# Optimization experiments

Measured on AMD Instinct MI355X. Metric: run time of the kernel, lower is better.

The kernel has to match this reference:

```python
import jax, jax.numpy as jnp
import numpy as np

N_NODES = 50000
N_EDGES = 600000
NUM_ENTITIES = 50000
EMBED = 128
HIDDEN = 128
NUM_TYPES = 16


def setup_inputs() -> dict:
    key = jax.random.key(0)
    ks = jax.random.split(key, 12)
    entity = jax.random.randint(ks[0], (N_NODES,), 0, NUM_ENTITIES, dtype=jnp.int64 if jax.config.jax_enable_x64 else jnp.int32)
    edge_index = jax.random.randint(ks[1], (2, N_EDGES), 0, N_NODES, dtype=jnp.int32)
    s = 1.0 / np.sqrt(EMBED)
    emb = jax.random.normal(ks[2], (NUM_ENTITIES, EMBED), jnp.float32)
    emb = emb.at[0].set(0.0)  # padding_idx=0
    W1_l = jax.random.uniform(ks[3], (EMBED, HIDDEN), jnp.float32, -s, s)
    b1 = jax.random.uniform(ks[4], (HIDDEN,), jnp.float32, -s, s)
    W1_r = jax.random.uniform(ks[5], (EMBED, HIDDEN), jnp.float32, -s, s)
    W2_l = jax.random.uniform(ks[6], (HIDDEN, HIDDEN), jnp.float32, -s, s)
    b2 = jax.random.uniform(ks[7], (HIDDEN,), jnp.float32, -s, s)
    W2_r = jax.random.uniform(ks[8], (HIDDEN, HIDDEN), jnp.float32, -s, s)
    Wc = jax.random.uniform(ks[9], (HIDDEN, NUM_TYPES), jnp.float32, -s, s)
    bc = jax.random.uniform(ks[10], (NUM_TYPES,), jnp.float32, -s, s)
    return {"entity": entity, "edge_index": edge_index, "emb": emb,
            "W1_l": W1_l, "b1": b1, "W1_r": W1_r,
            "W2_l": W2_l, "b2": b2, "W2_r": W2_r,
            "Wc": Wc, "bc": bc}


def _sage_conv(x, src, dst, Wl, bl, Wr):
    # PyG SAGEConv (aggr='mean'): out = lin_l(mean_{j->i} x_j) + lin_r(x_i)
    msgs = x[src]                                            # [E, D] gather
    agg = jax.ops.segment_sum(msgs, dst, num_segments=N_NODES)
    deg = jax.ops.segment_sum(jnp.ones((src.shape[0],), x.dtype), dst, num_segments=N_NODES)
    agg = agg / jnp.maximum(deg, 1.0)[:, None]               # mean; 0 for isolated nodes
    return agg @ Wl + bl + x @ Wr


def reference(entity, edge_index, emb, W1_l, b1, W1_r, W2_l, b2, W2_r, Wc, bc):
    src, dst = edge_index[0], edge_index[1]
    x = emb[entity]                                          # [N, 128] embedding lookup
    x = jax.nn.relu(_sage_conv(x, src, dst, W1_l, b1, W1_r))
    x = _sage_conv(x, src, dst, W2_l, b2, W2_r)
    return x @ Wc + bc                                       # [N, num_node_types]
```

## Files before the change

### kernel.cpp

```cpp
#include <hip/hip_runtime.h>

typedef _Float16 half4  __attribute__((ext_vector_type(4)));
typedef _Float16 half8  __attribute__((ext_vector_type(8)));
typedef float    f32x4  __attribute__((ext_vector_type(4)));

#define EC 768
#define CAP 4096
#define CHUNK 2048
#define CPAD 16
#define GA_PER 4

__device__ __forceinline__ void gather_unit(const int* __restrict__ ent,
                                            const float* __restrict__ emb,
                                            _Float16* __restrict__ X,
                                            int unit, int lt, int N) {
  int t = unit * 256 + lt;
  if (t >= N * 16) return;
  int node = t >> 4, g = t & 15;
  const float4* s = (const float4*)(emb + (long)ent[node] * 128 + g * 8);
  float4 a = s[0], c = s[1];
  half8 o;
  o[0] = (_Float16)a.x; o[1] = (_Float16)a.y; o[2] = (_Float16)a.z; o[3] = (_Float16)a.w;
  o[4] = (_Float16)c.x; o[5] = (_Float16)c.y; o[6] = (_Float16)c.z; o[7] = (_Float16)c.w;
  *(half8*)(X + (long)t * 8) = o;
}

__device__ __forceinline__ void pack_dev(const float* Wa, const float* Wb,
                                         _Float16* out, int NT, int ncols, int t) {
  int lane = t & 63, tile = t >> 6;
  int nt = tile % NT, kt = tile / NT;
  int n  = nt * 16 + (lane & 15);
  int kb = kt * 32 + (lane >> 4) * 8;
  half8 o;
#pragma unroll
  for (int j = 0; j < 8; ++j) {
    int k = kb + j;
    float w = (k < 128) ? Wa[k * ncols + n] : Wb[(k - 128) * ncols + n];
    o[j] = (_Float16)w;
  }
  *(half8*)(out + (long)t * 8) = o;
}

__global__ __launch_bounds__(256) void bucketA_k(
    const int* __restrict__ src, const int* __restrict__ dst,
    int* __restrict__ cur, int* __restrict__ buck,
    const int* __restrict__ ent, const float* __restrict__ emb, _Float16* __restrict__ X,
    const float* __restrict__ W1l, const float* __restrict__ W1r, _Float16* __restrict__ Wp1,
    const float* __restrict__ W2l, const float* __restrict__ W2r, const float* __restrict__ Wc,
    _Float16* __restrict__ Wz, const float* __restrict__ b2, const float* __restrict__ bc,
    float* __restrict__ bpr, int N, int E, int NA, int NBUCK, int IBA) {
  int b = blockIdx.x;
  if (b < IBA) {
    int grp = b / (GA_PER + 1), ph = b % (GA_PER + 1);
    if (ph != 0) { gather_unit(ent, emb, X, grp * GA_PER + ph - 1, threadIdx.x, N); return; }
    __shared__ int lbin[256], gbase[256];
    int tl = threadIdx.x;
    lbin[tl] = 0; __syncthreads();
    int e0 = grp * CHUNK;
    int pk[8], bn[8], lr[8];
    if (e0 + CHUNK <= E) {
      const int4* dp = (const int4*)(dst + e0 + tl * 8);
      const int4* sp = (const int4*)(src + e0 + tl * 8);
      int4 d0 = dp[0], d1 = dp[1], s0 = sp[0], s1 = sp[1];
      int dv[8] = {d0.x, d0.y, d0.z, d0.w, d1.x, d1.y, d1.z, d1.w};
      int sv[8] = {s0.x, s0.y, s0.z, s0.w, s1.x, s1.y, s1.z, s1.w};
#pragma unroll
      for (int k = 0; k < 8; ++k) {
        bn[k] = dv[k] >> 8;
        pk[k] = (sv[k] << 8) | (dv[k] & 255);
        lr[k] = atomicAdd(&lbin[bn[k]], 1);
      }
    } else {
#pragma unroll
      for (int k = 0; k < 8; ++k) {
        int e = e0 + tl * 8 + k;
        bn[k] = -1;
        if (e < E) {
          int d = dst[e];
          bn[k] = d >> 8;
          pk[k] = (src[e] << 8) | (d & 255);
          lr[k] = atomicAdd(&lbin[bn[k]], 1);
        }
      }
    }
    __syncthreads();
    gbase[tl] = (tl < NBUCK && lbin[tl]) ? atomicAdd(&cur[tl * CPAD], lbin[tl]) : 0;
    __syncthreads();
#pragma unroll
    for (int k = 0; k < 8; ++k) {
      if (bn[k] >= 0) {
        int idx = gbase[bn[k]] + lr[k];
        if (idx < CAP) buck[(long)bn[k] * CAP + idx] = pk[k];
      }
    }
  } else if (b < IBA + 16) {
    pack_dev(W1l, W1r, Wp1, 8, 128, (b - IBA) * 256 + threadIdx.x);
  } else if (b < IBA + 32) {
    int i = (b - IBA - 16) * 256 + threadIdx.x;
    int j = i & 7, lane = (i >> 3) & 63, tile = i >> 9;
    int nt = tile & 1, kt = tile >> 1;
    int k = kt * 32 + (lane >> 4) * 8 + j;
    int c = lane & 15;
    const float* W = nt ? W2r : W2l;
    float s = 0.f;
#pragma unroll 8
    for (int q = 0; q < 128; ++q) s += W[k * 128 + q] * Wc[q * 16 + c];
    Wz[i] = (_Float16)s;
  } else {
    int n = threadIdx.x;
    if (n < 16) {
      float s = bc[n];
      for (int k = 0; k < 128; ++k) s += b2[k] * Wc[k * 16 + n];
      bpr[n] = s;
    }
  }
}

__global__ __launch_bounds__(512) void bucketB_k(
    const int* __restrict__ cur, const int* __restrict__ buck,
    int* __restrict__ row_off, int* __restrict__ csr,
    const int* __restrict__ ent, const float* __restrict__ emb,
    _Float16* __restrict__ X, int goff, int N, int E, int NBUCK) {
  int B0 = blockIdx.x, tl = threadIdx.x;
  if (B0 >= NBUCK) {
    int unit = goff + (B0 - NBUCK) * 2 + (tl >> 8);
    gather_unit(ent, emb, X, unit, tl & 255, N);
    return;
  }
  __shared__ int sA[256], cnt[256], sB[256], run[256];
  if (tl < 256) sA[tl] = (tl < NBUCK) ? cur[tl * CPAD] : 0;
  if (tl < 256) cnt[tl] = 0;
  __syncthreads();
  for (int off = 1; off < 256; off <<= 1) {
    int a = (tl < 256) ? sA[tl] : 0;
    int bb = (tl >= off && tl < 256) ? sA[tl - off] : 0;
    __syncthreads();
    if (tl < 256) sA[tl] = a + bb;
    __syncthreads();
  }
  int bsz = cur[B0 * CPAD]; if (bsz > CAP) bsz = CAP;
  int ebase = sA[B0] - bsz;
  const int* bp = buck + (long)B0 * CAP;
  for (int i = tl; i < bsz; i += 512) atomicAdd(&cnt[bp[i] & 255], 1);
  __syncthreads();
  int cv = (tl < 256) ? cnt[tl] : 0;
  if (tl < 256) sB[tl] = cv;
  __syncthreads();
  for (int off = 1; off < 256; off <<= 1) {
    int a = (tl < 256) ? sB[tl] : 0;
    int bb = (tl >= off && tl < 256) ? sB[tl - off] : 0;
    __syncthreads();
    if (tl < 256) sB[tl] = a + bb;
    __syncthreads();
  }
  if (tl < 256) {
    int loff = sB[tl] - cv;
    int node = (B0 << 8) + tl;
    if (node < N) row_off[node] = ebase + loff;
    if (B0 == 0 && tl == 0) row_off[N] = E;
    run[tl] = loff;
  }
  __syncthreads();
  for (int i = tl; i < bsz; i += 512) {
    int w = bp[i];
    int r = atomicAdd(&run[w & 255], 1);
    csr[ebase + r] = w >> 8;
  }
}

__device__ __forceinline__ void agg_to_lds(const _Float16* __restrict__ X,
                                           const int* __restrict__ row_off,
                                           const int* __restrict__ csr,
                                           _Float16* ab, int* eidx,
                                           int row0, int M, int lane) {
  int nd_end = min(row0 + 16, M);
  int ebeg = row_off[row0 < M ? row0 : M - 1];
  int eend = row_off[nd_end];
  int cnt  = eend - ebeg;
  bool fits = (cnt <= EC);
  if (fits)
    for (int i = lane; i < cnt; i += 64) eidx[i] = csr[ebeg + i];
  int g = lane >> 4, j = lane & 15;
#pragma unroll
  for (int batch = 0; batch < 4; ++batch) {
    int node = row0 + batch * 4 + g;
    int nc = (node < M) ? node : M - 1;
    int beg = row_off[nc], end = row_off[nc + 1];
    half8 acc = (half8)(_Float16)0.f;
    if (fits) {
      const int* ix = eidx + (beg - ebeg);
      int n = end - beg;
#pragma unroll 8
      for (int e = 0; e < n; ++e) {
        half8 v = *(const half8*)(X + (long)ix[e] * 128 + j * 8);
        acc += v;
      }
    } else {
#pragma unroll 8
      for (int e = beg; e < end; ++e) {
        half8 v = *(const half8*)(X + (long)csr[e] * 128 + j * 8);
        acc += v;
      }
    }
    _Float16 inv = (_Float16)(1.f / fmaxf((float)(end - beg), 1.f));
    acc *= (half8)inv;
    *(half8*)(ab + (batch * 4 + g) * 136 + j * 8) = acc;
  }
}

__global__ __launch_bounds__(128) void gemm1z_k(const _Float16* __restrict__ X,
                                                const int* __restrict__ row_off,
                                                const int* __restrict__ csr,
                                                const _Float16* __restrict__ Bp,
                                                const float* __restrict__ bias,
                                                const _Float16* __restrict__ Bz,
                                                const float* __restrict__ bprime,
                                                _Float16* __restrict__ Zl,
                                                float* __restrict__ Pr, int M) {
  __shared__ _Float16 abuf[2][16 * 136];
  __shared__ int      ebuf[2][EC];
  int wave = threadIdx.x >> 6, lane = threadIdx.x & 63;
  _Float16* ab = abuf[wave];
  int row0 = blockIdx.x * 32 + wave * 16;
  agg_to_lds(X, row_off, csr, ab, ebuf[wave], row0, M, lane);
  int m = lane & 15, quad = lane >> 4;
  int arow = row0 + m; if (arow > M - 1) arow = M - 1;
  f32x4 acc[8];
#pragma unroll
  for (int i = 0; i < 8; ++i) acc[i] = (f32x4){0.f, 0.f, 0.f, 0.f};
#pragma unroll
  for (int kt = 0; kt < 8; ++kt) {
    half8 af = (kt < 4) ? *(const half8*)(ab + m * 136 + kt * 32 + quad * 8)
                        : *(const half8*)(X + (long)arow * 128 + (kt - 4) * 32 + quad * 8);
    __builtin_amdgcn_s_setprio(1);
#pragma unroll
    for (int nt = 0; nt < 8; ++nt) {
      half8 bf = *(const half8*)(Bp + ((long)(kt * 8 + nt) * 64 + lane) * 8);
      acc[nt] = __builtin_amdgcn_mfma_f32_16x16x32_f16(af, bf, acc[nt], 0, 0, 0);
    }
    __builtin_amdgcn_s_setprio(0);
  }
#pragma unroll
  for (int nt = 0; nt < 8; ++nt) {
    float bv = bias[nt * 16 + m];
#pragma unroll
    for (int r = 0; r < 4; ++r)
      ab[(quad * 4 + r) * 136 + nt * 16 + m] = (_Float16)fmaxf(acc[nt][r] + bv, 0.f);
  }
  f32x4 a0 = (f32x4){0.f, 0.f, 0.f, 0.f}, a1 = a0;
  __builtin_amdgcn_s_setprio(1);
#pragma unroll
  for (int kt = 0; kt < 4; ++kt) {
    half8 af = *(const half8*)(ab + m * 136 + kt * 32 + quad * 8);
    half8 b0 = *(const half8*)(Bz + ((long)(kt * 2 + 0) * 64 + lane) * 8);
    half8 b1 = *(const half8*)(Bz + ((long)(kt * 2 + 1) * 64 + lane) * 8);
    a0 = __builtin_amdgcn_mfma_f32_16x16x32_f16(af, b0, a0, 0, 0, 0);
    a1 = __builtin_amdgcn_mfma_f32_16x16x32_f16(af, b1, a1, 0, 0, 0);
  }
  __builtin_amdgcn_s_setprio(0);
  float bv = bprime[m];
#pragma unroll
  for (int r = 0; r < 4; ++r) {
    int orow = row0 + quad * 4 + r;
    if (orow < M) {
      Zl[(long)orow * 16 + m] = (_Float16)a0[r];
      Pr[(long)orow * 16 + m] = a1[r] + bv;
    }
  }
}

__global__ __launch_bounds__(256) void aggout_k(const _Float16* __restrict__ Zl,
                                                const float* __restrict__ Pr,
                                                const int* __restrict__ row_off,
                                                const int* __restrict__ csr,
                                                float* __restrict__ out, int M) {
  int t = blockIdx.x * 256 + threadIdx.x;
  int node = t >> 2, q = t & 3;
  if (node >= M) return;
  int beg = row_off[node], end = row_off[node + 1];
  float a0 = 0.f, a1 = 0.f, a2 = 0.f, a3 = 0.f;
#pragma unroll 8
  for (int e = beg; e < end; ++e) {
    half4 v = *(const half4*)(Zl + (long)csr[e] * 16 + q * 4);
    a0 += (float)v[0]; a1 += (float)v[1]; a2 += (float)v[2]; a3 += (float)v[3];
  }
  float inv = 1.f / fmaxf((float)(end - beg), 1.f);
  long o = (long)node * 16 + q * 4;
  const float4 pv = *(const float4*)(Pr + o);
  float4 ov;
  ov.x = a0 * inv + pv.x; ov.y = a1 * inv + pv.y;
  ov.z = a2 * inv + pv.z; ov.w = a3 * inv + pv.w;
  *(float4*)(out + o) = ov;
}

extern "C" void kernel_launch(void* const* d_in, const int* in_sizes, int n_in,
                              void* d_out, int out_size, void* d_ws, size_t ws_size,
                              hipStream_t stream) {
  const int N = in_sizes[0];
  const int E = in_sizes[1] / 2;
  const int*   entity = (const int*)d_in[0];
  const int*   e_src  = (const int*)d_in[1];
  const int*   e_dst  = e_src + E;
  const float* emb    = (const float*)d_in[2];
  const float* W1l    = (const float*)d_in[3];
  const float* b1     = (const float*)d_in[4];
  const float* W1r    = (const float*)d_in[5];
  const float* W2l    = (const float*)d_in[6];
  const float* b2     = (const float*)d_in[7];
  const float* W2r    = (const float*)d_in[8];
  const float* Wc     = (const float*)d_in[9];
  const float* bc     = (const float*)d_in[10];
  float* out = (float*)d_out;

  const int NBUCK = (N + 255) >> 8;

  char* p = (char*)d_ws;
  _Float16* x0  = (_Float16*)p; p += (size_t)N * 128 * 2;
  _Float16* Wp1 = (_Float16*)p; p += 256 * 128 * 2;
  _Float16* Wz  = (_Float16*)p; p += 128 * 32 * 2;
  float*    bpr = (float*)p;    p += 16 * 4;
  _Float16* Zl  = (_Float16*)p; p += (size_t)N * 16 * 2;
  float*    Pr  = (float*)p;    p += (size_t)N * 16 * 4;
  int* cur     = (int*)p; p += (size_t)NBUCK * CPAD * 4;
  int* row_off = (int*)p; p += (size_t)(N + 1) * 4;
  int* csr     = (int*)p; p += (size_t)E * 4;
  int* buck    = (int*)p; p += (size_t)NBUCK * CAP * 4;

  const int NA  = (E + CHUNK - 1) / CHUNK;
  const int GB  = (N * 16 + 255) / 256;
  const int IBA = (GA_PER + 1) * NA;
  int G1 = NA * GA_PER; if (G1 > GB) G1 = GB;
  const int G2 = GB - G1;
  const int BG = (G2 + 1) / 2;

  hipMemsetAsync(cur, 0, (size_t)NBUCK * CPAD * 4, stream);

  bucketA_k<<<IBA + 33, 256, 0, stream>>>(e_src, e_dst, cur, buck,
                                          entity, emb, x0, W1l, W1r, Wp1,
                                          W2l, W2r, Wc, Wz, b2, bc, bpr,
                                          N, E, NA, NBUCK, IBA);
  bucketB_k<<<NBUCK + BG, 512, 0, stream>>>(cur, buck, row_off, csr,
                                            entity, emb, x0, G1, N, E, NBUCK);
  gemm1z_k<<<(N + 31) / 32, 128, 0, stream>>>(x0, row_off, csr, Wp1, b1,
                                              Wz, bpr, Zl, Pr, N);
  aggout_k<<<(N * 4 + 255) / 256, 256, 0, stream>>>(Zl, Pr, row_off, csr, out, N);
}
```

Before: 156.1 us.

## Split gemm1z block work across four waves sharing LDS tiles

The fused aggregate+GEMM kernel now uses 256 threads per 32-row block instead of 128. Each of four waves aggregates 8 rows, then the waves form a 2x2 grid over rows and output columns for the MFMA stages. LDS tiles are shared through __syncthreads, and the ebuf region is reused for the hidden activations. This halves per-wave accumulator registers and gives more latency-hiding parallelism during the gather, at the cost of two block barriers.

```diff
diff --git a/kernel.cpp b/kernel.cpp
--- a/kernel.cpp
+++ b/kernel.cpp
@@ -168,22 +168,23 @@
   }
 }
 
-__device__ __forceinline__ void agg_to_lds(const _Float16* __restrict__ X,
-                                           const int* __restrict__ row_off,
-                                           const int* __restrict__ csr,
-                                           _Float16* ab, int* eidx,
-                                           int row0, int M, int lane) {
-  int nd_end = min(row0 + 16, M);
-  int ebeg = row_off[row0 < M ? row0 : M - 1];
-  int eend = row_off[nd_end];
+__device__ __forceinline__ void agg8(const _Float16* __restrict__ X,
+                                     const int* __restrict__ row_off,
+                                     const int* __restrict__ csr,
+                                     _Float16* ab,
+                                     int* eidx,
+                                     int rowbase, int M, int lane) {
+  int rb0 = rowbase < M ? rowbase : M - 1;
+  int rb1 = rowbase + 8; if (rb1 > M) rb1 = M;
+  int ebeg = row_off[rb0], eend = row_off[rb1];
   int cnt  = eend - ebeg;
   bool fits = (cnt <= EC);
   if (fits)
     for (int i = lane; i < cnt; i += 64) eidx[i] = csr[ebeg + i];
   int g = lane >> 4, j = lane & 15;
 #pragma unroll
-  for (int batch = 0; batch < 4; ++batch) {
-    int node = row0 + batch * 4 + g;
+  for (int batch = 0; batch < 2; ++batch) {
+    int node = rowbase + batch * 4 + g;
     int nc = (node < M) ? node : M - 1;
     int beg = row_off[nc], end = row_off[nc + 1];
     half8 acc = (half8)(_Float16)0.f;
@@ -208,7 +209,7 @@
   }
 }
 
-__global__ __launch_bounds__(128) void gemm1z_k(const _Float16* __restrict__ X,
+__global__ __launch_bounds__(256) void gemm1z_k(const _Float16* __restrict__ X,
                                                 const int* __restrict__ row_off,
                                                 const int* __restrict__ csr,
                                                 const _Float16* __restrict__ Bp,
@@ -217,54 +218,58 @@
                                                 const float* __restrict__ bprime,
                                                 _Float16* __restrict__ Zl,
                                                 float* __restrict__ Pr, int M) {
-  __shared__ _Float16 abuf[2][16 * 136];
-  __shared__ int      ebuf[2][EC];
+  __shared__ _Float16 abuf[32 * 136];
+  __shared__ int      ebuf_raw[4 * EC];
+  _Float16* h1b = (_Float16*)ebuf_raw;
   int wave = threadIdx.x >> 6, lane = threadIdx.x & 63;
-  _Float16* ab = abuf[wave];
-  int row0 = blockIdx.x * 32 + wave * 16;
-  agg_to_lds(X, row_off, csr, ab, ebuf[wave], row0, M, lane);
+  int row0 = blockIdx.x * 32;
+  agg8(X, row_off, csr, abuf + wave * 8 * 136, ebuf_raw + wave * EC,
+       row0 + wave * 8, M, lane);
+  __syncthreads();
   int m = lane & 15, quad = lane >> 4;
-  int arow = row0 + m; if (arow > M - 1) arow = M - 1;
-  f32x4 acc[8];
-#pragma unroll
-  for (int i = 0; i < 8; ++i) acc[i] = (f32x4){0.f, 0.f, 0.f, 0.f};
+  int r = wave >> 1, c = wave & 1;
+  int mrow = r * 16 + m;
+  int arow = row0 + mrow; if (arow > M - 1) arow = M - 1;
+  f32x4 acc[4];
+#pragma unroll
+  for (int i = 0; i < 4; ++i) acc[i] = (f32x4){0.f, 0.f, 0.f, 0.f};
 #pragma unroll
   for (int kt = 0; kt < 8; ++kt) {
-    half8 af = (kt < 4) ? *(const half8*)(ab + m * 136 + kt * 32 + quad * 8)
+    half8 af = (kt < 4) ? *(const half8*)(abuf + mrow * 136 + kt * 32 + quad * 8)
                         : *(const half8*)(X + (long)arow * 128 + (kt - 4) * 32 + quad * 8);
     __builtin_amdgcn_s_setprio(1);
 #pragma unroll
-    for (int nt = 0; nt < 8; ++nt) {
-      half8 bf = *(const half8*)(Bp + ((long)(kt * 8 + nt) * 64 + lane) * 8);
+    for (int nt = 0; nt < 4; ++nt) {
+      half8 bf = *(const half8*)(Bp + ((long)(kt * 8 + c * 4 + nt) * 64 + lane) * 8);
       acc[nt] = __builtin_amdgcn_mfma_f32_16x16x32_f16(af, bf, acc[nt], 0, 0, 0);
     }
     __builtin_amdgcn_s_setprio(0);
   }
 #pragma unroll
-  for (int nt = 0; nt < 8; ++nt) {
-    float bv = bias[nt * 16 + m];
-#pragma unroll
-    for (int r = 0; r < 4; ++r)
-      ab[(quad * 4 + r) * 136 + nt * 16 + m] = (_Float16)fmaxf(acc[nt][r] + bv, 0.f);
-  }
-  f32x4 a0 = (f32x4){0.f, 0.f, 0.f, 0.f}, a1 = a0;
+  for (int nt = 0; nt < 4; ++nt) {
+    float bv = bias[c * 64 + nt * 16 + m];
+#pragma unroll
+    for (int rr = 0; rr < 4; ++rr)
+      h1b[(r * 16 + quad * 4 + rr) * 136 + c * 64 + nt * 16 + m] =
+          (_Float16)fmaxf(acc[nt][rr] + bv, 0.f);
+  }
+  __syncthreads();
+  f32x4 a0 = (f32x4){0.f, 0.f, 0.f, 0.f};
   __builtin_amdgcn_s_setprio(1);
 #pragma unroll
   for (int kt = 0; kt < 4; ++kt) {
-    half8 af = *(const half8*)(ab + m * 136 + kt * 32 + quad * 8);
-    half8 b0 = *(const half8*)(Bz + ((long)(kt * 2 + 0) * 64 + lane) * 8);
-    half8 b1 = *(const half8*)(Bz + ((long)(kt * 2 + 1) * 64 + lane) * 8);
-    a0 = __builtin_amdgcn_mfma_f32_16x16x32_f16(af, b0, a0, 0, 0, 0);
-    a1 = __builtin_amdgcn_mfma_f32_16x16x32_f16(af, b1, a1, 0, 0, 0);
+    half8 af = *(const half8*)(h1b + mrow * 136 + kt * 32 + quad * 8);
+    half8 bf = *(const half8*)(Bz + ((long)(kt * 2 + c) * 64 + lane) * 8);
+    a0 = __builtin_amdgcn_mfma_f32_16x16x32_f16(af, bf, a0, 0, 0, 0);
   }
   __builtin_amdgcn_s_setprio(0);
   float bv = bprime[m];
 #pragma unroll
-  for (int r = 0; r < 4; ++r) {
-    int orow = row0 + quad * 4 + r;
+  for (int rr = 0; rr < 4; ++rr) {
+    int orow = row0 + r * 16 + quad * 4 + rr;
     if (orow < M) {
-      Zl[(long)orow * 16 + m] = (_Float16)a0[r];
-      Pr[(long)orow * 16 + m] = a1[r] + bv;
+      if (c == 0) Zl[(long)orow * 16 + m] = (_Float16)a0[rr];
+      else        Pr[(long)orow * 16 + m] = a0[rr] + bv;
     }
   }
 }
@@ -341,7 +346,7 @@
                                           N, E, NA, NBUCK, IBA);
   bucketB_k<<<NBUCK + BG, 512, 0, stream>>>(cur, buck, row_off, csr,
                                             entity, emb, x0, G1, N, E, NBUCK);
-  gemm1z_k<<<(N + 31) / 32, 128, 0, stream>>>(x0, row_off, csr, Wp1, b1,
+  gemm1z_k<<<(N + 31) / 32, 256, 0, stream>>>(x0, row_off, csr, Wp1, b1,
                                               Wz, bpr, Zl, Pr, N);
   aggout_k<<<(N * 4 + 255) / 256, 256, 0, stream>>>(Zl, Pr, row_off, csr, out, N);
 }
```

Measured after the change: 162.4 us. 4.0% more time.
